# Kernel optimization log

Hardware: AMD Instinct MI355X
Metric: run time of the kernel (lower is better)

The kernel has to match this reference:

```python
import jax, jax.numpy as jnp
import numpy as np

N_NODES = 50000
N_EDGES = 800000
NUM_FEATURES = 128
HIDDEN = 128
EMBED = 64
OUT_DIM = 1


def setup_inputs() -> dict:
    key = jax.random.key(0)
    ks = jax.random.split(key, 12)
    x = jax.random.normal(ks[0], (N_NODES, NUM_FEATURES), dtype=jnp.float32)
    edge_index = jax.random.randint(ks[1], (2, N_EDGES), 0, N_NODES, dtype=jnp.int64)

    def glorot(k, fan_in, fan_out):
        s = jnp.sqrt(6.0 / (fan_in + fan_out)).astype(jnp.float32)
        return jax.random.uniform(k, (fan_in, fan_out), jnp.float32, -s, s)

    return {
        "x": x,
        "edge_index": edge_index,
        "W1": glorot(ks[2], NUM_FEATURES, HIDDEN),
        "b1": jnp.zeros((HIDDEN,), jnp.float32),
        "Wh": glorot(ks[3], HIDDEN, HIDDEN),
        "bh": jnp.zeros((HIDDEN,), jnp.float32),
        "W2": glorot(ks[4], HIDDEN, EMBED),
        "b2": jnp.zeros((EMBED,), jnp.float32),
        "Wout": glorot(ks[5], EMBED, OUT_DIM),
        "bout": jnp.zeros((OUT_DIM,), jnp.float32),
    }


def _gcn_norm(edge_index, num_nodes):
    # Add self-loops, compute symmetric normalization deg^{-1/2} A_hat deg^{-1/2}
    loop = jnp.arange(num_nodes, dtype=edge_index.dtype)
    src = jnp.concatenate([edge_index[0], loop])
    dst = jnp.concatenate([edge_index[1], loop])
    deg = jax.ops.segment_sum(jnp.ones_like(dst, dtype=jnp.float32), dst,
                              num_segments=num_nodes)
    dis = jnp.where(deg > 0, jax.lax.rsqrt(jnp.maximum(deg, 1.0)), 0.0)
    norm = dis[src] * dis[dst]  # [E+N]
    return src, dst, norm


def _gcn_conv(h, W, b, src, dst, norm, num_nodes):
    h = h @ W  # linear transform first (PyG GCNConv)
    msg = h[src] * norm[:, None]  # gather + scale
    return jax.ops.segment_sum(msg, dst, num_segments=num_nodes) + b


def reference(x, edge_index, W1, b1, Wh, bh, W2, b2, Wout, bout):
    n = x.shape[0]
    src, dst, norm = _gcn_norm(edge_index, n)
    h = jax.nn.relu(_gcn_conv(x, W1, b1, src, dst, norm, n))  # dropout p=0 -> identity
    h = jax.nn.relu(_gcn_conv(h, Wh, bh, src, dst, norm, n))
    h = _gcn_conv(h, W2, b2, src, dst, norm, n)
    out = h @ Wout + bout
    return (out, h)
```

## Files before the change

kernel.cpp:

```cpp
#include <hip/hip_runtime.h>
#include <hip/hip_bf16.h>


#define N_NODES 50000
#define N_EDGES 800000
#define NBUCK 196
#define GB 196
#define EPB 4096

typedef __attribute__((ext_vector_type(8))) short short8;
typedef __attribute__((ext_vector_type(4))) float f32x4;

static __device__ __forceinline__ unsigned short f2bf(float f) {
    __hip_bfloat16 h = __float2bfloat16(f);
    return *reinterpret_cast<unsigned short*>(&h);
}
static __device__ __forceinline__ float bf2f(unsigned short u) {
    return __uint_as_float(((unsigned)u) << 16);
}


__global__ __launch_bounds__(256) void hist_kernel(const int* __restrict__ dstv,
                                                   int* __restrict__ H, int nE) {
    __shared__ int h[NBUCK];
    for (int i = threadIdx.x; i < NBUCK; i += 256) h[i] = 0;
    __syncthreads();
    int base = blockIdx.x * EPB;
#pragma unroll
    for (int i = 0; i < EPB / 256; ++i) {
        int e = base + i * 256 + threadIdx.x;
        if (e < nE) atomicAdd(&h[dstv[e] >> 8], 1);
    }
    __syncthreads();
    for (int i = threadIdx.x; i < NBUCK; i += 256)
        H[i * GB + blockIdx.x] = h[i];
}

__global__ __launch_bounds__(256) void scan1_kernel(int* __restrict__ H,
                                                    int* __restrict__ bsum) {
    __shared__ int s[256];
    int t = threadIdx.x;
    int k = blockIdx.x;
    int v = (t < GB) ? H[k * GB + t] : 0;
    s[t] = v;
    __syncthreads();
    for (int off = 1; off < 256; off <<= 1) {
        int u = (t >= off) ? s[t - off] : 0;
        __syncthreads();
        s[t] += u;
        __syncthreads();
    }
    if (t < GB) H[k * GB + t] = s[t] - v;
    if (t == 255) bsum[k] = s[255];
}

__global__ __launch_bounds__(256) void scan2_kernel(const int* __restrict__ bsum,
                                                    int* __restrict__ bstart,
                                                    int* __restrict__ rowoff_last) {
    __shared__ int s[256];
    int t = threadIdx.x;
    int v = (t < NBUCK) ? bsum[t] : 0;
    s[t] = v;
    __syncthreads();
    for (int off = 1; off < 256; off <<= 1) {
        int u = (t >= off) ? s[t - off] : 0;
        __syncthreads();
        s[t] += u;
        __syncthreads();
    }
    if (t < NBUCK) bstart[t] = s[t] - v;
    if (t == 0) {
        bstart[NBUCK] = N_EDGES;
        *rowoff_last = N_EDGES;
    }
}

__global__ __launch_bounds__(256) void partition_kernel(const int* __restrict__ srcv,
                                                        const int* __restrict__ dstv,
                                                        const int* __restrict__ H,
                                                        const int* __restrict__ bstart,
                                                        int2* __restrict__ P, int nE) {
    __shared__ int cur[NBUCK];
    for (int i = threadIdx.x; i < NBUCK; i += 256)
        cur[i] = bstart[i] + H[i * GB + blockIdx.x];
    __syncthreads();
    int base = blockIdx.x * EPB;
#pragma unroll
    for (int i = 0; i < EPB / 256; ++i) {
        int e = base + i * 256 + threadIdx.x;
        if (e < nE) {
            int d = dstv[e];
            int sv = srcv[e];
            int pos = atomicAdd(&cur[d >> 8], 1);
            P[pos] = make_int2(sv, d);
        }
    }
}

__global__ __launch_bounds__(256) void bucket_csr_kernel(const int2* __restrict__ P,
                                                         const int* __restrict__ bstart,
                                                         int* __restrict__ rowoff,
                                                         float* __restrict__ dis,
                                                         int* __restrict__ csr_src, int n) {
    __shared__ int cnt[256];
    __shared__ int s[256];
    __shared__ int cur[256];
    int t = threadIdx.x;
    int k = blockIdx.x;
    int ebeg = bstart[k], eend = bstart[k + 1];
    cnt[t] = 0;
    __syncthreads();
    for (int e = ebeg + t; e < eend; e += 256)
        atomicAdd(&cnt[P[e].y & 255], 1);
    __syncthreads();
    int myc = cnt[t];
    s[t] = myc;
    __syncthreads();
    for (int off = 1; off < 256; off <<= 1) {
        int v = (t >= off) ? s[t - off] : 0;
        __syncthreads();
        s[t] += v;
        __syncthreads();
    }
    int excl = s[t] - myc;
    int node = (k << 8) + t;
    if (node < n) {
        rowoff[node] = ebeg + excl;
        dis[node] = rsqrtf((float)(myc + 1));
    }
    cur[t] = ebeg + excl;
    __syncthreads();
    for (int e = ebeg + t; e < eend; e += 256) {
        int2 p = P[e];
        int pos = atomicAdd(&cur[p.y & 255], 1);
        csr_src[pos] = p.x;
    }
}

__global__ __launch_bounds__(256) void wprep_kernel(const float* __restrict__ W,
                                                    unsigned short* __restrict__ Whi,
                                                    unsigned short* __restrict__ Wlo,
                                                    int nout) {
    int t = blockIdx.x * 256 + threadIdx.x;
    if (t >= nout * 128) return;
    int col = t >> 7, k = t & 127;
    float v = W[(size_t)k * nout + col];
    unsigned short hi = f2bf(v);
    unsigned short lo = f2bf(v - bf2f(hi));
    Whi[(size_t)col * 128 + k] = hi;
    Wlo[(size_t)col * 128 + k] = lo;
}

template <int NOUT>
__global__ __launch_bounds__(256) void gemm_mfma_kernel(
    const float* __restrict__ A,
    const unsigned short* __restrict__ Wthi,
    const unsigned short* __restrict__ Wtlo,
    const float* __restrict__ scale,
    unsigned short* __restrict__ C, int M) {
    constexpr int LDK = 136;
    __shared__ unsigned short sAhi[64 * LDK];
    __shared__ unsigned short sAlo[64 * LDK];
    __shared__ unsigned short sBhi[64 * LDK];
    __shared__ unsigned short sBlo[64 * LDK];

    int tid = threadIdx.x;
    int Rbase = blockIdx.x * 64;
    int Cbase = blockIdx.y * 64;

    for (int i = tid; i < 64 * 32; i += 256) {
        int r = i >> 5, c4 = i & 31;
        int row = Rbase + r;
        float4 v = make_float4(0.f, 0.f, 0.f, 0.f);
        if (row < M) v = ((const float4*)(A + (size_t)row * 128))[c4];
        ushort4 hi, lo;
        hi.x = f2bf(v.x); lo.x = f2bf(v.x - bf2f(hi.x));
        hi.y = f2bf(v.y); lo.y = f2bf(v.y - bf2f(hi.y));
        hi.z = f2bf(v.z); lo.z = f2bf(v.z - bf2f(hi.z));
        hi.w = f2bf(v.w); lo.w = f2bf(v.w - bf2f(hi.w));
        *(ushort4*)(sAhi + r * LDK + c4 * 4) = hi;
        *(ushort4*)(sAlo + r * LDK + c4 * 4) = lo;
    }
    for (int i = tid; i < 64 * 32; i += 256) {
        int c = i >> 5, k4 = i & 31;
        *(ushort4*)(sBhi + c * LDK + k4 * 4) =
            *((const ushort4*)(Wthi + (size_t)(Cbase + c) * 128) + k4);
        *(ushort4*)(sBlo + c * LDK + k4 * 4) =
            *((const ushort4*)(Wtlo + (size_t)(Cbase + c) * 128) + k4);
    }
    __syncthreads();

    int w = tid >> 6, lane = tid & 63;
    int quad = lane >> 4, m = lane & 15;
    int r0 = (w & 1) * 32, c0 = (w >> 1) * 32;

    f32x4 z = {0.f, 0.f, 0.f, 0.f};
    f32x4 acc00 = z, acc01 = z, acc10 = z, acc11 = z;

#pragma unroll
    for (int ks = 0; ks < 4; ++ks) {
        int kof = ks * 32 + quad * 8;
        short8 ah0 = *(const short8*)(sAhi + (r0 + m) * LDK + kof);
        short8 ah1 = *(const short8*)(sAhi + (r0 + 16 + m) * LDK + kof);
        short8 al0 = *(const short8*)(sAlo + (r0 + m) * LDK + kof);
        short8 al1 = *(const short8*)(sAlo + (r0 + 16 + m) * LDK + kof);
        short8 bh0 = *(const short8*)(sBhi + (c0 + m) * LDK + kof);
        short8 bh1 = *(const short8*)(sBhi + (c0 + 16 + m) * LDK + kof);
        short8 bl0 = *(const short8*)(sBlo + (c0 + m) * LDK + kof);
        short8 bl1 = *(const short8*)(sBlo + (c0 + 16 + m) * LDK + kof);
        acc00 = __builtin_amdgcn_mfma_f32_16x16x32_bf16(ah0, bh0, acc00, 0, 0, 0);
        acc01 = __builtin_amdgcn_mfma_f32_16x16x32_bf16(ah0, bh1, acc01, 0, 0, 0);
        acc10 = __builtin_amdgcn_mfma_f32_16x16x32_bf16(ah1, bh0, acc10, 0, 0, 0);
        acc11 = __builtin_amdgcn_mfma_f32_16x16x32_bf16(ah1, bh1, acc11, 0, 0, 0);
        acc00 = __builtin_amdgcn_mfma_f32_16x16x32_bf16(ah0, bl0, acc00, 0, 0, 0);
        acc01 = __builtin_amdgcn_mfma_f32_16x16x32_bf16(ah0, bl1, acc01, 0, 0, 0);
        acc10 = __builtin_amdgcn_mfma_f32_16x16x32_bf16(ah1, bl0, acc10, 0, 0, 0);
        acc11 = __builtin_amdgcn_mfma_f32_16x16x32_bf16(ah1, bl1, acc11, 0, 0, 0);
        acc00 = __builtin_amdgcn_mfma_f32_16x16x32_bf16(al0, bh0, acc00, 0, 0, 0);
        acc01 = __builtin_amdgcn_mfma_f32_16x16x32_bf16(al0, bh1, acc01, 0, 0, 0);
        acc10 = __builtin_amdgcn_mfma_f32_16x16x32_bf16(al1, bh0, acc10, 0, 0, 0);
        acc11 = __builtin_amdgcn_mfma_f32_16x16x32_bf16(al1, bh1, acc11, 0, 0, 0);
    }

#pragma unroll
    for (int reg = 0; reg < 4; ++reg) {
        int row0g = Rbase + r0 + quad * 4 + reg;
        if (row0g < M) {
            float sc = scale[row0g];
            C[(size_t)row0g * NOUT + Cbase + c0 + m]      = f2bf(acc00[reg] * sc);
            C[(size_t)row0g * NOUT + Cbase + c0 + 16 + m] = f2bf(acc01[reg] * sc);
        }
        int row1g = row0g + 16;
        if (row1g < M) {
            float sc = scale[row1g];
            C[(size_t)row1g * NOUT + Cbase + c0 + m]      = f2bf(acc10[reg] * sc);
            C[(size_t)row1g * NOUT + Cbase + c0 + 16 + m] = f2bf(acc11[reg] * sc);
        }
    }
}

__global__ __launch_bounds__(256) void aggregate128_kernel(
    const int* __restrict__ rowoff, const int* __restrict__ csr_src,
    const float* __restrict__ dis, const unsigned short* __restrict__ tp,
    const float* __restrict__ bias, float* __restrict__ hout, int n) {
    int wid = (blockIdx.x * 256 + threadIdx.x) >> 6;
    int lane = threadIdx.x & 63;
    int n0 = wid * 2;
    if (n0 >= n) return;
    int n1 = n0 + 1;
    bool has1 = (n1 < n);
    const ushort2* base = (const ushort2*)tp + lane;

    float dd0 = dis[n0];
    int beg0 = rowoff[n0];
    int mid  = rowoff[n0 + 1];
    int end1 = has1 ? rowoff[n1 + 1] : mid;
    float dd1 = has1 ? dis[n1] : 0.f;

    ushort2 s0 = base[(size_t)n0 * 64];
    float a0x = bf2f(s0.x), a0y = bf2f(s0.y);
    float a1x = 0.f, a1y = 0.f;
    if (has1) {
        ushort2 s1 = base[(size_t)n1 * 64];
        a1x = bf2f(s1.x);
        a1y = bf2f(s1.y);
    }

    int i0 = beg0, i1 = mid;
    while (i0 + 4 <= mid && i1 + 4 <= end1) {
        int p0 = csr_src[i0], p1 = csr_src[i0 + 1], p2 = csr_src[i0 + 2], p3 = csr_src[i0 + 3];
        int q0 = csr_src[i1], q1 = csr_src[i1 + 1], q2 = csr_src[i1 + 2], q3 = csr_src[i1 + 3];
        ushort2 u0 = base[(size_t)p0 * 64], u1 = base[(size_t)p1 * 64];
        ushort2 u2 = base[(size_t)p2 * 64], u3 = base[(size_t)p3 * 64];
        ushort2 v0 = base[(size_t)q0 * 64], v1 = base[(size_t)q1 * 64];
        ushort2 v2 = base[(size_t)q2 * 64], v3 = base[(size_t)q3 * 64];
        a0x += (bf2f(u0.x) + bf2f(u1.x)) + (bf2f(u2.x) + bf2f(u3.x));
        a0y += (bf2f(u0.y) + bf2f(u1.y)) + (bf2f(u2.y) + bf2f(u3.y));
        a1x += (bf2f(v0.x) + bf2f(v1.x)) + (bf2f(v2.x) + bf2f(v3.x));
        a1y += (bf2f(v0.y) + bf2f(v1.y)) + (bf2f(v2.y) + bf2f(v3.y));
        i0 += 4;
        i1 += 4;
    }
    for (; i0 + 4 <= mid; i0 += 4) {
        int p0 = csr_src[i0], p1 = csr_src[i0 + 1], p2 = csr_src[i0 + 2], p3 = csr_src[i0 + 3];
        ushort2 u0 = base[(size_t)p0 * 64], u1 = base[(size_t)p1 * 64];
        ushort2 u2 = base[(size_t)p2 * 64], u3 = base[(size_t)p3 * 64];
        a0x += (bf2f(u0.x) + bf2f(u1.x)) + (bf2f(u2.x) + bf2f(u3.x));
        a0y += (bf2f(u0.y) + bf2f(u1.y)) + (bf2f(u2.y) + bf2f(u3.y));
    }
    for (; i0 < mid; ++i0) {
        ushort2 u = base[(size_t)csr_src[i0] * 64];
        a0x += bf2f(u.x);
        a0y += bf2f(u.y);
    }
    for (; i1 + 4 <= end1; i1 += 4) {
        int q0 = csr_src[i1], q1 = csr_src[i1 + 1], q2 = csr_src[i1 + 2], q3 = csr_src[i1 + 3];
        ushort2 v0 = base[(size_t)q0 * 64], v1 = base[(size_t)q1 * 64];
        ushort2 v2 = base[(size_t)q2 * 64], v3 = base[(size_t)q3 * 64];
        a1x += (bf2f(v0.x) + bf2f(v1.x)) + (bf2f(v2.x) + bf2f(v3.x));
        a1y += (bf2f(v0.y) + bf2f(v1.y)) + (bf2f(v2.y) + bf2f(v3.y));
    }
    for (; i1 < end1; ++i1) {
        ushort2 v = base[(size_t)csr_src[i1] * 64];
        a1x += bf2f(v.x);
        a1y += bf2f(v.y);
    }

    float2 b = ((const float2*)bias)[lane];
    float r0x = fmaxf(a0x * dd0 + b.x, 0.f);
    float r0y = fmaxf(a0y * dd0 + b.y, 0.f);
    ((float2*)hout)[(size_t)n0 * 64 + lane] = make_float2(r0x, r0y);
    if (has1) {
        float r1x = fmaxf(a1x * dd1 + b.x, 0.f);
        float r1y = fmaxf(a1y * dd1 + b.y, 0.f);
        ((float2*)hout)[(size_t)n1 * 64 + lane] = make_float2(r1x, r1y);
    }
}

__global__ __launch_bounds__(256) void aggregate64_head_kernel(
    const int* __restrict__ rowoff, const int* __restrict__ csr_src,
    const float* __restrict__ dis, const unsigned short* __restrict__ tp,
    const float* __restrict__ bias, const float* __restrict__ Wout,
    const float* __restrict__ bout, float* __restrict__ hout,
    float* __restrict__ out, int n) {
    int node = (blockIdx.x * 256 + threadIdx.x) >> 6;
    int lane = threadIdx.x & 63;
    if (node >= n) return;
    float dd = dis[node];
    const unsigned short* base = tp + lane;
    float acc = bf2f(base[(size_t)node * 64]);
    int beg = rowoff[node], end = rowoff[node + 1];
    int i = beg;
    for (; i + 4 <= end; i += 4) {
        int s0 = csr_src[i], s1 = csr_src[i + 1], s2 = csr_src[i + 2], s3 = csr_src[i + 3];
        float v0 = bf2f(base[(size_t)s0 * 64]);
        float v1 = bf2f(base[(size_t)s1 * 64]);
        float v2 = bf2f(base[(size_t)s2 * 64]);
        float v3 = bf2f(base[(size_t)s3 * 64]);
        acc += (v0 + v1) + (v2 + v3);
    }
    for (; i < end; ++i) acc += bf2f(base[(size_t)csr_src[i] * 64]);
    acc = acc * dd + bias[lane];
    hout[(size_t)node * 64 + lane] = acc;
    float p = acc * Wout[lane];
#pragma unroll
    for (int off = 32; off > 0; off >>= 1) p += __shfl_down(p, off);
    if (lane == 0) out[node] = p + bout[0];
}

extern "C" void kernel_launch(void* const* d_in, const int* in_sizes, int n_in,
                              void* d_out, int out_size, void* d_ws, size_t ws_size,
                              hipStream_t stream) {
    const float* x    = (const float*)d_in[0];
    const int*   ei   = (const int*)d_in[1];
    const float* W1   = (const float*)d_in[2];
    const float* b1   = (const float*)d_in[3];
    const float* Wh   = (const float*)d_in[4];
    const float* bh   = (const float*)d_in[5];
    const float* W2   = (const float*)d_in[6];
    const float* b2   = (const float*)d_in[7];
    const float* Wout = (const float*)d_in[8];
    const float* bout = (const float*)d_in[9];

    const int N = N_NODES;
    const int E = N_EDGES;
    const int* srcv = ei;
    const int* dstv = ei + E;

    float* out  = (float*)d_out;
    float* hout = (float*)d_out + N;

    char* ws = (char*)d_ws;
    int*   H       = (int*)ws;                          ws += sizeof(int) * NBUCK * GB;
    int*   bsum    = (int*)ws;                          ws += sizeof(int) * NBUCK;
    int*   bstart  = (int*)ws;                          ws += sizeof(int) * (NBUCK + 1);
    int*   rowoff  = (int*)ws;                          ws += sizeof(int) * (N + 1);
    int2*  P       = (int2*)ws;                         ws += sizeof(int2) * E;
    int*   csr_src = (int*)ws;                          ws += sizeof(int) * E;
    float* dis     = (float*)ws;                        ws += sizeof(float) * N;
    unsigned short* W1thi = (unsigned short*)ws;        ws += sizeof(unsigned short) * 128 * 128;
    unsigned short* W1tlo = (unsigned short*)ws;        ws += sizeof(unsigned short) * 128 * 128;
    unsigned short* Whthi = (unsigned short*)ws;        ws += sizeof(unsigned short) * 128 * 128;
    unsigned short* Whtlo = (unsigned short*)ws;        ws += sizeof(unsigned short) * 128 * 128;
    unsigned short* W2thi = (unsigned short*)ws;        ws += sizeof(unsigned short) * 64 * 128;
    unsigned short* W2tlo = (unsigned short*)ws;        ws += sizeof(unsigned short) * 64 * 128;
    unsigned short* bufT  = (unsigned short*)ws;        ws += sizeof(unsigned short) * (size_t)N * 128;
    float* bufH    = (float*)ws;

    wprep_kernel<<<(128 * 128 + 255) / 256, 256, 0, stream>>>(W1, W1thi, W1tlo, 128);
    wprep_kernel<<<(128 * 128 + 255) / 256, 256, 0, stream>>>(Wh, Whthi, Whtlo, 128);
    wprep_kernel<<<(64 * 128 + 255) / 256, 256, 0, stream>>>(W2, W2thi, W2tlo, 64);

    hist_kernel<<<GB, 256, 0, stream>>>(dstv, H, E);
    scan1_kernel<<<NBUCK, 256, 0, stream>>>(H, bsum);
    scan2_kernel<<<1, 256, 0, stream>>>(bsum, bstart, rowoff + N);
    partition_kernel<<<GB, 256, 0, stream>>>(srcv, dstv, H, bstart, P, E);
    bucket_csr_kernel<<<NBUCK, 256, 0, stream>>>(P, bstart, rowoff, dis, csr_src, N);

    const int aggBlocks = ((N + 1) / 2 * 64 + 255) / 256;
    const int gemmRows = (N + 63) / 64;

    gemm_mfma_kernel<128><<<dim3(gemmRows, 2), 256, 0, stream>>>(x, W1thi, W1tlo, dis, bufT, N);
    aggregate128_kernel<<<aggBlocks, 256, 0, stream>>>(rowoff, csr_src, dis, bufT, b1, bufH, N);

    gemm_mfma_kernel<128><<<dim3(gemmRows, 2), 256, 0, stream>>>(bufH, Whthi, Whtlo, dis, bufT, N);
    aggregate128_kernel<<<aggBlocks, 256, 0, stream>>>(rowoff, csr_src, dis, bufT, bh, bufH, N);

    gemm_mfma_kernel<64><<<dim3(gemmRows, 1), 256, 0, stream>>>(bufH, W2thi, W2tlo, dis, bufT, N);
    aggregate64_head_kernel<<<((size_t)N * 64 + 255) / 256, 256, 0, stream>>>(
        rowoff, csr_src, dis, bufT, b2, Wout, bout, hout, out, N);
}
```

Before: 310.3 us.

## Widen aggregation gathers, load GEMM weights to registers, merge weight prep launches

The three weight-prep launches become one kernel that reads W coalesced. The GEMM now loads B fragments straight from global memory into registers instead of staging them in shared memory, which halves LDS use. Both aggregation kernels split each wave into two halves that take alternating edges, with each lane gathering 8-byte (or 4-byte) row chunks, and the halves are combined with a cross-half shuffle. The 64-wide head kernel now handles two nodes per wave, so it launches half as many blocks. The cost is more register pressure in the GEMM and extra shuffles in the aggregations.

```diff
diff --git a/kernel.cpp b/kernel.cpp
--- a/kernel.cpp
+++ b/kernel.cpp
@@ -137,18 +137,25 @@
     }
 }
 
-__global__ __launch_bounds__(256) void wprep_kernel(const float* __restrict__ W,
-                                                    unsigned short* __restrict__ Whi,
-                                                    unsigned short* __restrict__ Wlo,
-                                                    int nout) {
+__global__ __launch_bounds__(256) void wprep_all_kernel(
+    const float* __restrict__ W1, const float* __restrict__ Wh, const float* __restrict__ W2,
+    unsigned short* __restrict__ W1hi, unsigned short* __restrict__ W1lo,
+    unsigned short* __restrict__ Whhi, unsigned short* __restrict__ Whlo,
+    unsigned short* __restrict__ W2hi, unsigned short* __restrict__ W2lo) {
     int t = blockIdx.x * 256 + threadIdx.x;
-    if (t >= nout * 128) return;
-    int col = t >> 7, k = t & 127;
-    float v = W[(size_t)k * nout + col];
+    const float* W;
+    unsigned short *Hi, *Lo;
+    int nout, lt;
+    if (t < 16384)      { W = W1; Hi = W1hi; Lo = W1lo; nout = 128; lt = t; }
+    else if (t < 32768) { W = Wh; Hi = Whhi; Lo = Whlo; nout = 128; lt = t - 16384; }
+    else if (t < 40960) { W = W2; Hi = W2hi; Lo = W2lo; nout = 64;  lt = t - 32768; }
+    else return;
+    int col = lt % nout, k = lt / nout;
+    float v = W[lt];
     unsigned short hi = f2bf(v);
     unsigned short lo = f2bf(v - bf2f(hi));
-    Whi[(size_t)col * 128 + k] = hi;
-    Wlo[(size_t)col * 128 + k] = lo;
+    Hi[(size_t)col * 128 + k] = hi;
+    Lo[(size_t)col * 128 + k] = lo;
 }
 
 template <int NOUT>
@@ -161,12 +168,23 @@
     constexpr int LDK = 136;
     __shared__ unsigned short sAhi[64 * LDK];
     __shared__ unsigned short sAlo[64 * LDK];
-    __shared__ unsigned short sBhi[64 * LDK];
-    __shared__ unsigned short sBlo[64 * LDK];
 
     int tid = threadIdx.x;
+    int w = tid >> 6, lane = tid & 63;
+    int quad = lane >> 4, m = lane & 15;
     int Rbase = blockIdx.x * 64;
     int Cbase = blockIdx.y * 64;
+    int r0 = (w & 1) * 32, c0 = (w >> 1) * 32;
+
+    short8 bh[4][2], bl[4][2];
+#pragma unroll
+    for (int ks = 0; ks < 4; ++ks)
+#pragma unroll
+        for (int g = 0; g < 2; ++g) {
+            size_t off = (size_t)(Cbase + c0 + g * 16 + m) * 128 + ks * 32 + quad * 8;
+            bh[ks][g] = *(const short8*)(Wthi + off);
+            bl[ks][g] = *(const short8*)(Wtlo + off);
+        }
 
     for (int i = tid; i < 64 * 32; i += 256) {
         int r = i >> 5, c4 = i & 31;
@@ -181,18 +199,7 @@
         *(ushort4*)(sAhi + r * LDK + c4 * 4) = hi;
         *(ushort4*)(sAlo + r * LDK + c4 * 4) = lo;
     }
-    for (int i = tid; i < 64 * 32; i += 256) {
-        int c = i >> 5, k4 = i & 31;
-        *(ushort4*)(sBhi + c * LDK + k4 * 4) =
-            *((const ushort4*)(Wthi + (size_t)(Cbase + c) * 128) + k4);
-        *(ushort4*)(sBlo + c * LDK + k4 * 4) =
-            *((const ushort4*)(Wtlo + (size_t)(Cbase + c) * 128) + k4);
-    }
-    __syncthreads();
-
-    int w = tid >> 6, lane = tid & 63;
-    int quad = lane >> 4, m = lane & 15;
-    int r0 = (w & 1) * 32, c0 = (w >> 1) * 32;
+    __syncthreads();
 
     f32x4 z = {0.f, 0.f, 0.f, 0.f};
     f32x4 acc00 = z, acc01 = z, acc10 = z, acc11 = z;
@@ -204,22 +211,18 @@
         short8 ah1 = *(const short8*)(sAhi + (r0 + 16 + m) * LDK + kof);
         short8 al0 = *(const short8*)(sAlo + (r0 + m) * LDK + kof);
         short8 al1 = *(const short8*)(sAlo + (r0 + 16 + m) * LDK + kof);
-        short8 bh0 = *(const short8*)(sBhi + (c0 + m) * LDK + kof);
-        short8 bh1 = *(const short8*)(sBhi + (c0 + 16 + m) * LDK + kof);
-        short8 bl0 = *(const short8*)(sBlo + (c0 + m) * LDK + kof);
-        short8 bl1 = *(const short8*)(sBlo + (c0 + 16 + m) * LDK + kof);
-        acc00 = __builtin_amdgcn_mfma_f32_16x16x32_bf16(ah0, bh0, acc00, 0, 0, 0);
-        acc01 = __builtin_amdgcn_mfma_f32_16x16x32_bf16(ah0, bh1, acc01, 0, 0, 0);
-        acc10 = __builtin_amdgcn_mfma_f32_16x16x32_bf16(ah1, bh0, acc10, 0, 0, 0);
-        acc11 = __builtin_amdgcn_mfma_f32_16x16x32_bf16(ah1, bh1, acc11, 0, 0, 0);
-        acc00 = __builtin_amdgcn_mfma_f32_16x16x32_bf16(ah0, bl0, acc00, 0, 0, 0);
-        acc01 = __builtin_amdgcn_mfma_f32_16x16x32_bf16(ah0, bl1, acc01, 0, 0, 0);
-        acc10 = __builtin_amdgcn_mfma_f32_16x16x32_bf16(ah1, bl0, acc10, 0, 0, 0);
-        acc11 = __builtin_amdgcn_mfma_f32_16x16x32_bf16(ah1, bl1, acc11, 0, 0, 0);
-        acc00 = __builtin_amdgcn_mfma_f32_16x16x32_bf16(al0, bh0, acc00, 0, 0, 0);
-        acc01 = __builtin_amdgcn_mfma_f32_16x16x32_bf16(al0, bh1, acc01, 0, 0, 0);
-        acc10 = __builtin_amdgcn_mfma_f32_16x16x32_bf16(al1, bh0, acc10, 0, 0, 0);
-        acc11 = __builtin_amdgcn_mfma_f32_16x16x32_bf16(al1, bh1, acc11, 0, 0, 0);
+        acc00 = __builtin_amdgcn_mfma_f32_16x16x32_bf16(ah0, bh[ks][0], acc00, 0, 0, 0);
+        acc01 = __builtin_amdgcn_mfma_f32_16x16x32_bf16(ah0, bh[ks][1], acc01, 0, 0, 0);
+        acc10 = __builtin_amdgcn_mfma_f32_16x16x32_bf16(ah1, bh[ks][0], acc10, 0, 0, 0);
+        acc11 = __builtin_amdgcn_mfma_f32_16x16x32_bf16(ah1, bh[ks][1], acc11, 0, 0, 0);
+        acc00 = __builtin_amdgcn_mfma_f32_16x16x32_bf16(ah0, bl[ks][0], acc00, 0, 0, 0);
+        acc01 = __builtin_amdgcn_mfma_f32_16x16x32_bf16(ah0, bl[ks][1], acc01, 0, 0, 0);
+        acc10 = __builtin_amdgcn_mfma_f32_16x16x32_bf16(ah1, bl[ks][0], acc10, 0, 0, 0);
+        acc11 = __builtin_amdgcn_mfma_f32_16x16x32_bf16(ah1, bl[ks][1], acc11, 0, 0, 0);
+        acc00 = __builtin_amdgcn_mfma_f32_16x16x32_bf16(al0, bh[ks][0], acc00, 0, 0, 0);
+        acc01 = __builtin_amdgcn_mfma_f32_16x16x32_bf16(al0, bh[ks][1], acc01, 0, 0, 0);
+        acc10 = __builtin_amdgcn_mfma_f32_16x16x32_bf16(al1, bh[ks][0], acc10, 0, 0, 0);
+        acc11 = __builtin_amdgcn_mfma_f32_16x16x32_bf16(al1, bh[ks][1], acc11, 0, 0, 0);
     }
 
 #pragma unroll
@@ -245,75 +248,62 @@
     const float* __restrict__ bias, float* __restrict__ hout, int n) {
     int wid = (blockIdx.x * 256 + threadIdx.x) >> 6;
     int lane = threadIdx.x & 63;
+    int h = lane >> 5, lc = lane & 31;
     int n0 = wid * 2;
     if (n0 >= n) return;
     int n1 = n0 + 1;
     bool has1 = (n1 < n);
-    const ushort2* base = (const ushort2*)tp + lane;
-
-    float dd0 = dis[n0];
-    int beg0 = rowoff[n0];
-    int mid  = rowoff[n0 + 1];
+
+    float a0[4] = {0.f, 0.f, 0.f, 0.f};
+    float a1[4] = {0.f, 0.f, 0.f, 0.f};
+
+#define ROW128(node) (*((const ushort4*)(tp + (size_t)(node) * 128) + lc))
+#define ACC(a, u) { a[0] += bf2f(u.x); a[1] += bf2f(u.y); a[2] += bf2f(u.z); a[3] += bf2f(u.w); }
+
+    if (h == 0) { ushort4 u = ROW128(n0); ACC(a0, u); }
+    else if (has1) { ushort4 u = ROW128(n1); ACC(a1, u); }
+
+    int mid = rowoff[n0 + 1];
+    int i0 = rowoff[n0] + h;
+    int i1 = mid + h;
     int end1 = has1 ? rowoff[n1 + 1] : mid;
-    float dd1 = has1 ? dis[n1] : 0.f;
-
-    ushort2 s0 = base[(size_t)n0 * 64];
-    float a0x = bf2f(s0.x), a0y = bf2f(s0.y);
-    float a1x = 0.f, a1y = 0.f;
-    if (has1) {
-        ushort2 s1 = base[(size_t)n1 * 64];
-        a1x = bf2f(s1.x);
-        a1y = bf2f(s1.y);
-    }
-
-    int i0 = beg0, i1 = mid;
-    while (i0 + 4 <= mid && i1 + 4 <= end1) {
-        int p0 = csr_src[i0], p1 = csr_src[i0 + 1], p2 = csr_src[i0 + 2], p3 = csr_src[i0 + 3];
-        int q0 = csr_src[i1], q1 = csr_src[i1 + 1], q2 = csr_src[i1 + 2], q3 = csr_src[i1 + 3];
-        ushort2 u0 = base[(size_t)p0 * 64], u1 = base[(size_t)p1 * 64];
-        ushort2 u2 = base[(size_t)p2 * 64], u3 = base[(size_t)p3 * 64];
-        ushort2 v0 = base[(size_t)q0 * 64], v1 = base[(size_t)q1 * 64];
-        ushort2 v2 = base[(size_t)q2 * 64], v3 = base[(size_t)q3 * 64];
-        a0x += (bf2f(u0.x) + bf2f(u1.x)) + (bf2f(u2.x) + bf2f(u3.x));
-        a0y += (bf2f(u0.y) + bf2f(u1.y)) + (bf2f(u2.y) + bf2f(u3.y));
-        a1x += (bf2f(v0.x) + bf2f(v1.x)) + (bf2f(v2.x) + bf2f(v3.x));
-        a1y += (bf2f(v0.y) + bf2f(v1.y)) + (bf2f(v2.y) + bf2f(v3.y));
-        i0 += 4;
-        i1 += 4;
-    }
-    for (; i0 + 4 <= mid; i0 += 4) {
-        int p0 = csr_src[i0], p1 = csr_src[i0 + 1], p2 = csr_src[i0 + 2], p3 = csr_src[i0 + 3];
-        ushort2 u0 = base[(size_t)p0 * 64], u1 = base[(size_t)p1 * 64];
-        ushort2 u2 = base[(size_t)p2 * 64], u3 = base[(size_t)p3 * 64];
-        a0x += (bf2f(u0.x) + bf2f(u1.x)) + (bf2f(u2.x) + bf2f(u3.x));
-        a0y += (bf2f(u0.y) + bf2f(u1.y)) + (bf2f(u2.y) + bf2f(u3.y));
-    }
-    for (; i0 < mid; ++i0) {
-        ushort2 u = base[(size_t)csr_src[i0] * 64];
-        a0x += bf2f(u.x);
-        a0y += bf2f(u.y);
-    }
-    for (; i1 + 4 <= end1; i1 += 4) {
-        int q0 = csr_src[i1], q1 = csr_src[i1 + 1], q2 = csr_src[i1 + 2], q3 = csr_src[i1 + 3];
-        ushort2 v0 = base[(size_t)q0 * 64], v1 = base[(size_t)q1 * 64];
-        ushort2 v2 = base[(size_t)q2 * 64], v3 = base[(size_t)q3 * 64];
-        a1x += (bf2f(v0.x) + bf2f(v1.x)) + (bf2f(v2.x) + bf2f(v3.x));
-        a1y += (bf2f(v0.y) + bf2f(v1.y)) + (bf2f(v2.y) + bf2f(v3.y));
-    }
-    for (; i1 < end1; ++i1) {
-        ushort2 v = base[(size_t)csr_src[i1] * 64];
-        a1x += bf2f(v.x);
-        a1y += bf2f(v.y);
-    }
-
-    float2 b = ((const float2*)bias)[lane];
-    float r0x = fmaxf(a0x * dd0 + b.x, 0.f);
-    float r0y = fmaxf(a0y * dd0 + b.y, 0.f);
-    ((float2*)hout)[(size_t)n0 * 64 + lane] = make_float2(r0x, r0y);
-    if (has1) {
-        float r1x = fmaxf(a1x * dd1 + b.x, 0.f);
-        float r1y = fmaxf(a1y * dd1 + b.y, 0.f);
-        ((float2*)hout)[(size_t)n1 * 64 + lane] = make_float2(r1x, r1y);
+
+    while (i0 + 2 < mid && i1 + 2 < end1) {
+        int s0a = csr_src[i0], s0b = csr_src[i0 + 2];
+        int s1a = csr_src[i1], s1b = csr_src[i1 + 2];
+        ushort4 u0 = ROW128(s0a), u1 = ROW128(s0b);
+        ushort4 v0 = ROW128(s1a), v1 = ROW128(s1b);
+        ACC(a0, u0); ACC(a0, u1);
+        ACC(a1, v0); ACC(a1, v1);
+        i0 += 4; i1 += 4;
+    }
+    for (; i0 < mid; i0 += 2) { ushort4 u = ROW128(csr_src[i0]); ACC(a0, u); }
+    for (; i1 < end1; i1 += 2) { ushort4 v = ROW128(csr_src[i1]); ACC(a1, v); }
+#undef ROW128
+
+#pragma unroll
+    for (int j = 0; j < 4; ++j) {
+        a0[j] += __shfl_xor(a0[j], 32);
+        a1[j] += __shfl_xor(a1[j], 32);
+    }
+
+    float4 b = ((const float4*)bias)[lc];
+    if (h == 0) {
+        float dd = dis[n0];
+        float4 r;
+        r.x = fmaxf(a0[0] * dd + b.x, 0.f);
+        r.y = fmaxf(a0[1] * dd + b.y, 0.f);
+        r.z = fmaxf(a0[2] * dd + b.z, 0.f);
+        r.w = fmaxf(a0[3] * dd + b.w, 0.f);
+        ((float4*)(hout + (size_t)n0 * 128))[lc] = r;
+    } else if (has1) {
+        float dd = dis[n1];
+        float4 r;
+        r.x = fmaxf(a1[0] * dd + b.x, 0.f);
+        r.y = fmaxf(a1[1] * dd + b.y, 0.f);
+        r.z = fmaxf(a1[2] * dd + b.z, 0.f);
+        r.w = fmaxf(a1[3] * dd + b.w, 0.f);
+        ((float4*)(hout + (size_t)n1 * 128))[lc] = r;
     }
 }
 
@@ -323,29 +313,63 @@
     const float* __restrict__ bias, const float* __restrict__ Wout,
     const float* __restrict__ bout, float* __restrict__ hout,
     float* __restrict__ out, int n) {
-    int node = (blockIdx.x * 256 + threadIdx.x) >> 6;
+    int wid = (blockIdx.x * 256 + threadIdx.x) >> 6;
     int lane = threadIdx.x & 63;
-    if (node >= n) return;
-    float dd = dis[node];
-    const unsigned short* base = tp + lane;
-    float acc = bf2f(base[(size_t)node * 64]);
-    int beg = rowoff[node], end = rowoff[node + 1];
-    int i = beg;
-    for (; i + 4 <= end; i += 4) {
-        int s0 = csr_src[i], s1 = csr_src[i + 1], s2 = csr_src[i + 2], s3 = csr_src[i + 3];
-        float v0 = bf2f(base[(size_t)s0 * 64]);
-        float v1 = bf2f(base[(size_t)s1 * 64]);
-        float v2 = bf2f(base[(size_t)s2 * 64]);
-        float v3 = bf2f(base[(size_t)s3 * 64]);
-        acc += (v0 + v1) + (v2 + v3);
-    }
-    for (; i < end; ++i) acc += bf2f(base[(size_t)csr_src[i] * 64]);
-    acc = acc * dd + bias[lane];
-    hout[(size_t)node * 64 + lane] = acc;
-    float p = acc * Wout[lane];
-#pragma unroll
-    for (int off = 32; off > 0; off >>= 1) p += __shfl_down(p, off);
-    if (lane == 0) out[node] = p + bout[0];
+    int h = lane >> 5, lc = lane & 31;
+    int n0 = wid * 2;
+    if (n0 >= n) return;
+    int n1 = n0 + 1;
+    bool has1 = (n1 < n);
+
+    float a0[2] = {0.f, 0.f};
+    float a1[2] = {0.f, 0.f};
+
+#define ROW64(node) (*((const ushort2*)(tp + (size_t)(node) * 64) + lc))
+#define ACC2(a, u) { a[0] += bf2f(u.x); a[1] += bf2f(u.y); }
+
+    if (h == 0) { ushort2 u = ROW64(n0); ACC2(a0, u); }
+    else if (has1) { ushort2 u = ROW64(n1); ACC2(a1, u); }
+
+    int mid = rowoff[n0 + 1];
+    int i0 = rowoff[n0] + h;
+    int i1 = mid + h;
+    int end1 = has1 ? rowoff[n1 + 1] : mid;
+
+    while (i0 + 2 < mid && i1 + 2 < end1) {
+        int s0a = csr_src[i0], s0b = csr_src[i0 + 2];
+        int s1a = csr_src[i1], s1b = csr_src[i1 + 2];
+        ushort2 u0 = ROW64(s0a), u1 = ROW64(s0b);
+        ushort2 v0 = ROW64(s1a), v1 = ROW64(s1b);
+        ACC2(a0, u0); ACC2(a0, u1);
+        ACC2(a1, v0); ACC2(a1, v1);
+        i0 += 4; i1 += 4;
+    }
+    for (; i0 < mid; i0 += 2) { ushort2 u = ROW64(csr_src[i0]); ACC2(a0, u); }
+    for (; i1 < end1; i1 += 2) { ushort2 v = ROW64(csr_src[i1]); ACC2(a1, v); }
+#undef ROW64
+
+#pragma unroll
+    for (int j = 0; j < 2; ++j) {
+        a0[j] += __shfl_xor(a0[j], 32);
+        a1[j] += __shfl_xor(a1[j], 32);
+    }
+
+    int node = h ? n1 : n0;
+    float* ap = h ? a1 : a0;
+    bool valid = (h == 0) || has1;
+    float2 hv = make_float2(0.f, 0.f);
+    if (valid) {
+        float dd = dis[node];
+        float2 b = ((const float2*)bias)[lc];
+        hv.x = ap[0] * dd + b.x;
+        hv.y = ap[1] * dd + b.y;
+        ((float2*)(hout + (size_t)node * 64))[lc] = hv;
+    }
+    float2 wv = ((const float2*)Wout)[lc];
+    float p = valid ? (hv.x * wv.x + hv.y * wv.y) : 0.f;
+#pragma unroll
+    for (int off = 16; off > 0; off >>= 1) p += __shfl_down(p, off);
+    if (lc == 0 && valid) out[node] = p + bout[0];
 }
 
 extern "C" void kernel_launch(void* const* d_in, const int* in_sizes, int n_in,
@@ -387,9 +411,7 @@
     unsigned short* bufT  = (unsigned short*)ws;        ws += sizeof(unsigned short) * (size_t)N * 128;
     float* bufH    = (float*)ws;
 
-    wprep_kernel<<<(128 * 128 + 255) / 256, 256, 0, stream>>>(W1, W1thi, W1tlo, 128);
-    wprep_kernel<<<(128 * 128 + 255) / 256, 256, 0, stream>>>(Wh, Whthi, Whtlo, 128);
-    wprep_kernel<<<(64 * 128 + 255) / 256, 256, 0, stream>>>(W2, W2thi, W2tlo, 64);
+    wprep_all_kernel<<<160, 256, 0, stream>>>(W1, Wh, W2, W1thi, W1tlo, Whthi, Whtlo, W2thi, W2tlo);
 
     hist_kernel<<<GB, 256, 0, stream>>>(dstv, H, E);
     scan1_kernel<<<NBUCK, 256, 0, stream>>>(H, bsum);
@@ -407,6 +429,6 @@
     aggregate128_kernel<<<aggBlocks, 256, 0, stream>>>(rowoff, csr_src, dis, bufT, bh, bufH, N);
 
     gemm_mfma_kernel<64><<<dim3(gemmRows, 1), 256, 0, stream>>>(bufH, W2thi, W2tlo, dis, bufT, N);
-    aggregate64_head_kernel<<<((size_t)N * 64 + 255) / 256, 256, 0, stream>>>(
+    aggregate64_head_kernel<<<aggBlocks, 256, 0, stream>>>(
         rowoff, csr_src, dis, bufT, b2, Wout, bout, hout, out, N);
 }
```

Result: faster. 303.2 us (-2.3%).
